# Performance work log

Hardware: AMD Instinct MI355X
Metric: run time of the kernel (lower is better)

## Reference

```python
import jax, jax.numpy as jnp
import numpy as np
from jax import lax

B, TIN, N, TOUT, C = 8, 168, 1500, 24, 16
EMB, ALPHA, BETA, TOPK, DEPTH = 16, 1.5, 0.2, 12, 2
KERNELS = (2, 3, 6, 7)


def setup_inputs() -> dict:
    key = jax.random.key(0)
    ks = jax.random.split(key, 32)
    def rn(k, shape, scale=0.1):
        return jax.random.normal(k, shape, jnp.float32) * scale
    inp = {"x": jax.random.normal(ks[0], (B, TIN, N, 1), jnp.float32)}
    inp["pw"], inp["pb"] = rn(ks[1], (C, 1)), rn(ks[2], (C,))
    branch = C // len(KERNELS)
    for i, k in enumerate(KERNELS):
        inp[f"tw{k}"] = rn(ks[3 + 2 * i], (branch, C, 1, k))
        inp[f"tb{k}"] = rn(ks[4 + 2 * i], (branch,))
    inp["e1"], inp["e2"] = rn(ks[11], (N, EMB), 1.0), rn(ks[12], (N, EMB), 1.0)
    inp["gw1"], inp["gb1"] = rn(ks[13], (EMB, EMB)), rn(ks[14], (EMB,))
    inp["gw2"], inp["gb2"] = rn(ks[15], (EMB, EMB)), rn(ks[16], (EMB,))
    inp["mw"], inp["mb"] = rn(ks[17], (C, (DEPTH + 1) * C)), rn(ks[18], (C,))
    inp["rw1"], inp["rb1"] = rn(ks[19], (C, C)), rn(ks[20], (C,))
    inp["rw2"], inp["rb2"] = rn(ks[21], (TOUT, C)), rn(ks[22], (TOUT,))
    return inp


def _conv1x1(h, w, b):
    # h: [B, Cin, N, T], w: [Cout, Cin], b: [Cout]
    return jnp.einsum('bint,oi->bont', h, w) + b[None, :, None, None]


def _forward(x, pw, pb, tw2, tb2, tw3, tb3, tw6, tb6, tw7, tb7,
             e1, e2, gw1, gb1, gw2, gb2, mw, mb, rw1, rb1, rw2, rb2):
    h = jnp.transpose(x, (0, 3, 2, 1))                      # [B,1,N,TIN]
    h = _conv1x1(h, pw, pb)                                 # [B,C,N,TIN]
    # dilated inception: branches with kernels (2,3,6,7), truncate to shortest
    tlen = TIN - max(KERNELS) + 1
    outs = []
    for w, b in ((tw2, tb2), (tw3, tb3), (tw6, tb6), (tw7, tb7)):
        o = lax.conv_general_dilated(h, w, (1, 1), 'VALID',
                                     dimension_numbers=('NCHW', 'OIHW', 'NCHW'))
        outs.append(o[..., -tlen:] + b[None, :, None, None])
    h = jax.nn.relu(jnp.concatenate(outs, axis=1))          # [B,C,N,tlen]
    # adaptive top-k graph learning
    m1 = jnp.tanh(ALPHA * (e1 @ gw1 + gb1))
    m2 = jnp.tanh(ALPHA * (e2 @ gw2 + gb2))
    a = jax.nn.relu(jnp.tanh(ALPHA * (m1 @ m2.T - m2 @ m1.T)))  # [N,N]
    _, idx = lax.top_k(a, TOPK)
    mask = jnp.zeros((N, N), jnp.float32).at[jnp.arange(N)[:, None], idx].set(1.0)
    adj = a * mask
    # mix-hop graph convolution with row-normalized (A + I)
    adj = adj + jnp.eye(N, dtype=jnp.float32)
    adj = adj / jnp.sum(adj, axis=1, keepdims=True)
    hin = h
    hops = [h]
    for _ in range(DEPTH):
        h = BETA * hin + (1.0 - BETA) * jnp.einsum('bcwt,vw->bcvt', h, adj)
        hops.append(h)
    ho = jnp.concatenate(hops, axis=1)                      # [B,(D+1)C,N,tlen]
    h = jax.nn.relu(_conv1x1(ho, mw, mb))                   # [B,C,N,tlen]
    # dropout -> identity at inference
    r = jax.nn.relu(_conv1x1(h, rw1, rb1))
    y = _conv1x1(r, rw2, rb2)                               # [B,TOUT,N,tlen]
    return jnp.mean(y, axis=-1)                             # [B,TOUT,N]


def reference(x, pw, pb, tw2, tb2, tw3, tb3, tw6, tb6, tw7, tb7,
              e1, e2, gw1, gb1, gw2, gb2, mw, mb, rw1, rb1, rw2, rb2):
    return _forward(x, pw, pb, tw2, tb2, tw3, tb3, tw6, tb6, tw7, tb7,
                    e1, e2, gw1, gb1, gw2, gb2, mw, mb, rw1, rb1, rw2, rb2)
```

## Files before the change

kernel.cpp:

```cpp
#include <hip/hip_runtime.h>

#define BB 8
#define TIN 168
#define NN 1500
#define TOUTC 24
#define TLEN 162
#define NG 32
#define NTH 768
#define SN 2
#define TOPKK 12
#define NTILE 94
#define NPAD 1504

#define OFF_M1   0
#define OFF_M2   24000
#define OFF_EW   48000
#define OFF_EB   48112
#define OFF_ADJW 48128
#define OFF_ADJI 67628
#define OFF_FR   87128
#define OFF_S16  88664
#define OFF_PART 280664

typedef __attribute__((ext_vector_type(8))) short short8;
typedef __attribute__((ext_vector_type(4))) float v4f;

__device__ __forceinline__ unsigned short f2bf(float f) {
    unsigned int u = __float_as_uint(f);
    unsigned int r = (u + 0x7fffu + ((u >> 16) & 1u)) >> 16;
    return (unsigned short)r;
}
__device__ __forceinline__ unsigned int pack2(float lo, float hi) {
    return (unsigned int)f2bf(lo) | ((unsigned int)f2bf(hi) << 16);
}
__device__ __forceinline__ float unlo(unsigned int u) { return __uint_as_float(u << 16); }
__device__ __forceinline__ float unhi(unsigned int u) { return __uint_as_float(u & 0xffff0000u); }
__device__ __forceinline__ float bf2f(unsigned short s) { return __uint_as_float(((unsigned int)s) << 16); }

__device__ __forceinline__ short8 as_s8(uint4 u) { union { uint4 a; short8 b; } c; c.a = u; return c.b; }
__device__ __forceinline__ uint4 zf_u4(v4f f)    { union { v4f a; uint4 b; } c; c.a = f; return c.b; }

__global__ __launch_bounds__(256) void prep_kernel(
    const float* __restrict__ e1, const float* __restrict__ e2,
    const float* __restrict__ gw1, const float* __restrict__ gb1,
    const float* __restrict__ gw2, const float* __restrict__ gb2,
    const float* __restrict__ pw, const float* __restrict__ pb,
    const float* __restrict__ tw2, const float* __restrict__ tb2,
    const float* __restrict__ tw3, const float* __restrict__ tb3,
    const float* __restrict__ tw6, const float* __restrict__ tb6,
    const float* __restrict__ tw7, const float* __restrict__ tb7,
    const float* __restrict__ mw, const float* __restrict__ rw1,
    float* __restrict__ ws)
{
    int n = blockIdx.x * blockDim.x + threadIdx.x;
    if (n < NN) {
        float a1[16], a2[16];
        #pragma unroll
        for (int o = 0; o < 16; ++o) { a1[o] = gb1[o]; a2[o] = gb2[o]; }
        #pragma unroll
        for (int i = 0; i < 16; ++i) {
            float u = e1[n*16+i], v = e2[n*16+i];
            #pragma unroll
            for (int o = 0; o < 16; ++o) {
                a1[o] += u * gw1[i*16+o];
                a2[o] += v * gw2[i*16+o];
            }
        }
        #pragma unroll
        for (int o = 0; o < 16; ++o) {
            ws[OFF_M1 + n*16+o] = tanhf(1.5f*a1[o]);
            ws[OFF_M2 + n*16+o] = tanhf(1.5f*a2[o]);
        }
    }
    if (blockIdx.x == 0 && threadIdx.x < 16) {
        int c = threadIdx.x;
        int br = c >> 2, oc = c & 3;
        const float* tw; const float* tb; int k;
        if (br == 0)      { tw = tw2; tb = tb2; k = 2; }
        else if (br == 1) { tw = tw3; tb = tb3; k = 3; }
        else if (br == 2) { tw = tw6; tb = tb6; k = 6; }
        else              { tw = tw7; tb = tb7; k = 7; }
        for (int d = 0; d < 7; ++d) ws[OFF_EW + c*7 + d] = 0.f;
        float ebv = tb[oc];
        for (int j = 0; j < k; ++j) {
            float s = 0.f, sb = 0.f;
            for (int ic = 0; ic < 16; ++ic) {
                float w = tw[(oc*16+ic)*k + j];
                s  += w * pw[ic];
                sb += w * pb[ic];
            }
            ws[OFF_EW + c*7 + (7-k+j)] = s;
            ebv += sb;
        }
        ws[OFF_EB + c] = ebv;
    }
    if (blockIdx.x == 1 && threadIdx.x < 64) {
        int lane = threadIdx.x;
        int m = lane & 15, q = lane >> 4;
        unsigned short* frw = (unsigned short*)(ws + OFF_FR);
        for (int mat = 0; mat < 3; ++mat) {
            for (int j = 0; j < 8; ++j) {
                int k = q*8 + j;
                float s;
                if (mat == 0) s = (k < 16) ? mw[m*48+k] + 0.2f*(mw[m*48+16+k] + mw[m*48+32+k])
                                           : 0.8f*mw[m*48+16+(k-16)] + 0.16f*mw[m*48+32+(k-16)];
                else if (mat == 1) s = (k < 16) ? 0.64f*mw[m*48+32+k] : 0.f;
                else               s = (k < 16) ? rw1[m*16+k] : 0.f;
                unsigned short hi = f2bf(s);
                unsigned short lo = f2bf(s - bf2f(hi));
                frw[(mat*2+0)*512 + lane*8 + j] = hi;
                frw[(mat*2+1)*512 + lane*8 + j] = lo;
            }
        }
    }
}

__global__ __launch_bounds__(256) void graph_kernel(
    const float* __restrict__ m1, const float* __restrict__ m2,
    float* __restrict__ adjw, int* __restrict__ adji)
{
    int v = blockIdx.x;
    int tid = threadIdx.x;
    __shared__ float wv4[4];
    __shared__ int   wi4[4];
    __shared__ int   bcast_i;
    __shared__ float m1v[16], m2v[16];
    if (tid < 16) { m1v[tid] = m1[v*16+tid]; m2v[tid] = m2[v*16+tid]; }
    __syncthreads();
    const float4* m1f = (const float4*)m1;
    const float4* m2f = (const float4*)m2;
    float sreg[6];
    #pragma unroll
    for (int u = 0; u < 6; ++u) {
        int j = tid + 256*u;
        float a = -1.f;
        if (j < NN) {
            float d = 0.f;
            #pragma unroll
            for (int q = 0; q < 4; ++q) {
                float4 r2 = m2f[j*4+q];
                float4 r1 = m1f[j*4+q];
                d += m1v[4*q+0]*r2.x - m2v[4*q+0]*r1.x;
                d += m1v[4*q+1]*r2.y - m2v[4*q+1]*r1.y;
                d += m1v[4*q+2]*r2.z - m2v[4*q+2]*r1.z;
                d += m1v[4*q+3]*r2.w - m2v[4*q+3]*r1.w;
            }
            float t = tanhf(1.5f*d);
            a = t > 0.f ? t : 0.f;
        }
        sreg[u] = a;
    }
    float lb = -1.f; int li = NN;
    #pragma unroll
    for (int u = 0; u < 6; ++u) {
        int j = tid + 256*u;
        if (j < NN && sreg[u] > lb) { lb = sreg[u]; li = j; }
    }
    const int wid = tid >> 6;
    for (int it = 0; it < TOPKK; ++it) {
        float bv = lb; int bi = li;
        #pragma unroll
        for (int off = 32; off > 0; off >>= 1) {
            float ov = __shfl_down(bv, off);
            int   oi = __shfl_down(bi, off);
            if (ov > bv || (ov == bv && oi < bi)) { bv = ov; bi = oi; }
        }
        if ((tid & 63) == 0) { wv4[wid] = bv; wi4[wid] = bi; }
        __syncthreads();
        if (tid == 0) {
            #pragma unroll
            for (int w = 1; w < 4; ++w) {
                float ov = wv4[w]; int oi = wi4[w];
                if (ov > bv || (ov == bv && oi < bi)) { bv = ov; bi = oi; }
            }
            adjw[v*13+it] = bv;
            adji[v*13+it] = bi;
            bcast_i = bi;
        }
        __syncthreads();
        int win = bcast_i;
        if (li == win) {
            #pragma unroll
            for (int u = 0; u < 6; ++u)
                if (tid + 256*u == win) sreg[u] = -1.f;
            lb = -1.f; li = NN;
            #pragma unroll
            for (int u = 0; u < 6; ++u) {
                int j = tid + 256*u;
                if (j < NN && sreg[u] > lb) { lb = sreg[u]; li = j; }
            }
        }
    }
    if (tid == 0) {
        float s = 1.f;
        #pragma unroll
        for (int it = 0; it < TOPKK; ++it) s += adjw[v*13+it];
        float inv = 1.f/s;
        #pragma unroll
        for (int it = 0; it < TOPKK; ++it) adjw[v*13+it] *= inv;
        adji[v*13+12] = v;
        adjw[v*13+12] = inv;
    }
}

__device__ __forceinline__ short8 ldfrag(const unsigned short* fr, int plane, int lane) {
    const uint4* p = (const uint4*)(fr + plane*512);
    return as_s8(p[lane]);
}

__global__ __launch_bounds__(NTH, 3) void main_kernel(
    const float* __restrict__ x,
    const float* __restrict__ ew, const float* __restrict__ eb,
    const float* __restrict__ adjw, const int* __restrict__ adji,
    const unsigned short* __restrict__ fr,
    float* __restrict__ part,
    const float* __restrict__ mb, const float* __restrict__ rb1)
{
    __shared__ uint4 feat[4][NPAD];
    __shared__ uint4 qp2[2][NPAD];

    const int tid = threadIdx.x;
    const int lane = tid & 63;
    const int wid = tid >> 6;
    const int b = blockIdx.x >> 5;
    const int g = blockIdx.x & 31;
    const int t0 = (g*TLEN) >> 5;
    const int t1 = ((g+1)*TLEN) >> 5;
    float* partBG = part + (size_t)(b*NG + g)*NN*16;

    for (int t = t0; t < t1; ++t) {
        #pragma unroll 1
        for (int s = 0; s < SN; ++s) {
            int v = tid + NTH*s;
            if (v < NN) {
                float xv[7];
                #pragma unroll
                for (int d = 0; d < 7; ++d) xv[d] = x[(b*TIN + t + d)*NN + v];
                float h[16];
                #pragma unroll
                for (int c = 0; c < 16; ++c) {
                    float a = eb[c];
                    #pragma unroll
                    for (int d = 0; d < 7; ++d) a += ew[c*7+d]*xv[d];
                    h[c] = a > 0.f ? a : 0.f;
                }
                feat[0][v] = make_uint4(pack2(h[0],h[1]), pack2(h[2],h[3]), pack2(h[4],h[5]), pack2(h[6],h[7]));
                feat[1][v] = make_uint4(pack2(h[8],h[9]), pack2(h[10],h[11]), pack2(h[12],h[13]), pack2(h[14],h[15]));
            }
        }
        __syncthreads();
        #pragma unroll 1
        for (int s = 0; s < SN; ++s) {
            int v = tid + NTH*s;
            if (v < NN) {
                float u1[16];
                #pragma unroll
                for (int c = 0; c < 16; ++c) u1[c] = 0.f;
                int base = v*13;
                #pragma unroll
                for (int j = 0; j < 13; ++j) {
                    int nb = adji[base+j];
                    float w = adjw[base+j];
                    uint4 b0 = feat[0][nb], b1 = feat[1][nb];
                    unsigned int uu[8] = {b0.x,b0.y,b0.z,b0.w,b1.x,b1.y,b1.z,b1.w};
                    #pragma unroll
                    for (int i = 0; i < 8; ++i) { u1[2*i] += w*unlo(uu[i]); u1[2*i+1] += w*unhi(uu[i]); }
                }
                feat[2][v] = make_uint4(pack2(u1[0],u1[1]), pack2(u1[2],u1[3]), pack2(u1[4],u1[5]), pack2(u1[6],u1[7]));
                feat[3][v] = make_uint4(pack2(u1[8],u1[9]), pack2(u1[10],u1[11]), pack2(u1[12],u1[13]), pack2(u1[14],u1[15]));
            }
        }
        __syncthreads();
        {
            short8 a1h = ldfrag(fr, 0, lane), a1l = ldfrag(fr, 1, lane);
            short8 a2h = ldfrag(fr, 2, lane), a2l = ldfrag(fr, 3, lane);
            const int n0 = lane & 15, q = lane >> 4;
            ushort4* qpH = (ushort4*)qp2;
            #pragma unroll 1
            for (int T = wid; T < NTILE; T += 12) {
                int n = T*16 + n0;
                short8 bf  = as_s8(feat[q][n]);
                short8 b2f = as_s8(feat[2 + (q & 1)][n]);
                v4f z = {0.f,0.f,0.f,0.f}, p = {0.f,0.f,0.f,0.f};
                z = __builtin_amdgcn_mfma_f32_16x16x32_bf16(a1h, bf, z, 0, 0, 0);
                z = __builtin_amdgcn_mfma_f32_16x16x32_bf16(a1l, bf, z, 0, 0, 0);
                p = __builtin_amdgcn_mfma_f32_16x16x32_bf16(a2h, b2f, p, 0, 0, 0);
                p = __builtin_amdgcn_mfma_f32_16x16x32_bf16(a2l, b2f, p, 0, 0, 0);
                feat[q][n] = zf_u4(z);
                ushort4 pp;
                pp.x = f2bf(p[0]); pp.y = f2bf(p[1]); pp.z = f2bf(p[2]); pp.w = f2bf(p[3]);
                qpH[(q >> 1)*(NPAD*2) + n*2 + (q & 1)] = pp;
            }
        }
        __syncthreads();
        #pragma unroll 1
        for (int s = 0; s < SN; ++s) {
            int v = tid + NTH*s;
            if (v < NN) {
                float y[16];
                #pragma unroll
                for (int qq = 0; qq < 4; ++qq) {
                    uint4 zz = feat[qq][v];
                    y[qq*4+0] = mb[qq*4+0] + __uint_as_float(zz.x);
                    y[qq*4+1] = mb[qq*4+1] + __uint_as_float(zz.y);
                    y[qq*4+2] = mb[qq*4+2] + __uint_as_float(zz.z);
                    y[qq*4+3] = mb[qq*4+3] + __uint_as_float(zz.w);
                }
                int base = v*13;
                #pragma unroll
                for (int j = 0; j < 13; ++j) {
                    int nb = adji[base+j];
                    float w = adjw[base+j];
                    uint4 p0 = qp2[0][nb], p1 = qp2[1][nb];
                    unsigned int uu[8] = {p0.x,p0.y,p0.z,p0.w,p1.x,p1.y,p1.z,p1.w};
                    #pragma unroll
                    for (int i = 0; i < 8; ++i) { y[2*i] += w*unlo(uu[i]); y[2*i+1] += w*unhi(uu[i]); }
                }
                #pragma unroll
                for (int o = 0; o < 16; ++o) y[o] = y[o] > 0.f ? y[o] : 0.f;
                feat[0][v] = make_uint4(pack2(y[0],y[1]), pack2(y[2],y[3]), pack2(y[4],y[5]), pack2(y[6],y[7]));
                feat[1][v] = make_uint4(pack2(y[8],y[9]), pack2(y[10],y[11]), pack2(y[12],y[13]), pack2(y[14],y[15]));
                feat[2][v] = make_uint4(0,0,0,0);
                feat[3][v] = make_uint4(0,0,0,0);
            }
        }
        __syncthreads();
        {
            short8 a3h = ldfrag(fr, 4, lane), a3l = ldfrag(fr, 5, lane);
            const int n0 = lane & 15, q = lane >> 4;
            float rb[4];
            #pragma unroll
            for (int r = 0; r < 4; ++r) rb[r] = rb1[q*4+r];
            #pragma unroll 1
            for (int T = wid; T < NTILE; T += 12) {
                int n = T*16 + n0;
                short8 bf = as_s8(feat[q][n]);
                v4f acc = {0.f,0.f,0.f,0.f};
                acc = __builtin_amdgcn_mfma_f32_16x16x32_bf16(a3h, bf, acc, 0, 0, 0);
                acc = __builtin_amdgcn_mfma_f32_16x16x32_bf16(a3l, bf, acc, 0, 0, 0);
                if (n < NN) {
                    float r0 = acc[0]+rb[0], r1 = acc[1]+rb[1], r2 = acc[2]+rb[2], r3 = acc[3]+rb[3];
                    r0 = r0 > 0.f ? r0 : 0.f;  r1 = r1 > 0.f ? r1 : 0.f;
                    r2 = r2 > 0.f ? r2 : 0.f;  r3 = r3 > 0.f ? r3 : 0.f;
                    float4* pp = (float4*)(partBG + (size_t)n*16 + q*4);
                    if (t == t0) {
                        *pp = make_float4(r0, r1, r2, r3);
                    } else {
                        float4 o = *pp;
                        *pp = make_float4(o.x+r0, o.y+r1, o.z+r2, o.w+r3);
                    }
                }
            }
        }
        __syncthreads();
    }
}

__global__ __launch_bounds__(256) void reduce1_kernel(const float* __restrict__ part,
                                                      float* __restrict__ s16buf)
{
    int idx = blockIdx.x*256 + threadIdx.x;
    if (idx >= BB*NN*16) return;
    int c = idx & 15;
    int rest = idx >> 4;
    int v = rest % NN;
    int b = rest / NN;
    float s = 0.f;
    #pragma unroll
    for (int g = 0; g < NG; ++g)
        s += part[((size_t)(b*NG + g)*NN + v)*16 + c];
    s16buf[idx] = s * (1.0f/TLEN);
}

__global__ __launch_bounds__(256) void reduce2_kernel(const float* __restrict__ s16buf,
                                                      const float* __restrict__ rw2,
                                                      const float* __restrict__ rb2,
                                                      float* __restrict__ out)
{
    int idx = blockIdx.x*256 + threadIdx.x;
    if (idx >= BB*NN) return;
    int v = idx % NN;
    int b = idx / NN;
    const float4* sp = (const float4*)(s16buf + (size_t)idx*16);
    float4 s0 = sp[0], s1 = sp[1], s2 = sp[2], s3 = sp[3];
    float s16[16] = {s0.x,s0.y,s0.z,s0.w, s1.x,s1.y,s1.z,s1.w,
                     s2.x,s2.y,s2.z,s2.w, s3.x,s3.y,s3.z,s3.w};
    #pragma unroll
    for (int o = 0; o < TOUTC; ++o) {
        float a = rb2[o];
        #pragma unroll
        for (int c = 0; c < 16; ++c) a += rw2[o*16+c]*s16[c];
        out[(b*TOUTC + o)*NN + v] = a;
    }
}

extern "C" void kernel_launch(void* const* d_in, const int* in_sizes, int n_in,
                              void* d_out, int out_size, void* d_ws, size_t ws_size,
                              hipStream_t stream)
{
    const float* x   = (const float*)d_in[0];
    const float* pw  = (const float*)d_in[1];
    const float* pb  = (const float*)d_in[2];
    const float* tw2 = (const float*)d_in[3];
    const float* tb2 = (const float*)d_in[4];
    const float* tw3 = (const float*)d_in[5];
    const float* tb3 = (const float*)d_in[6];
    const float* tw6 = (const float*)d_in[7];
    const float* tb6 = (const float*)d_in[8];
    const float* tw7 = (const float*)d_in[9];
    const float* tb7 = (const float*)d_in[10];
    const float* e1  = (const float*)d_in[11];
    const float* e2  = (const float*)d_in[12];
    const float* gw1 = (const float*)d_in[13];
    const float* gb1 = (const float*)d_in[14];
    const float* gw2 = (const float*)d_in[15];
    const float* gb2 = (const float*)d_in[16];
    const float* mw  = (const float*)d_in[17];
    const float* mb  = (const float*)d_in[18];
    const float* rw1 = (const float*)d_in[19];
    const float* rb1 = (const float*)d_in[20];
    const float* rw2 = (const float*)d_in[21];
    const float* rb2 = (const float*)d_in[22];
    float* ws  = (float*)d_ws;
    float* out = (float*)d_out;

    prep_kernel<<<(NN + 255)/256, 256, 0, stream>>>(e1,e2,gw1,gb1,gw2,gb2,pw,pb,
                                                    tw2,tb2,tw3,tb3,tw6,tb6,tw7,tb7,
                                                    mw, rw1, ws);
    graph_kernel<<<NN, 256, 0, stream>>>(ws + OFF_M1, ws + OFF_M2,
                                         ws + OFF_ADJW, (int*)ws + OFF_ADJI);
    main_kernel<<<BB*NG, NTH, 0, stream>>>(x, ws + OFF_EW, ws + OFF_EB,
                                           ws + OFF_ADJW, (const int*)ws + OFF_ADJI,
                                           (const unsigned short*)(ws + OFF_FR),
                                           ws + OFF_PART, mb, rb1);
    reduce1_kernel<<<(BB*NN*16 + 255)/256, 256, 0, stream>>>(ws + OFF_PART, ws + OFF_S16);
    reduce2_kernel<<<(BB*NN + 255)/256, 256, 0, stream>>>(ws + OFF_S16, rw2, rb2, out);
}
```

Measured before the change: 299.7 us.

## Fuse second hop into final MFMA tile loop and double-buffer input features

Restructures the main kernel's per-timestep pipeline. The input-projection features for the next timestep are computed into an alternate shared buffer, and the second-hop aggregation is folded into the tile loop that feeds the final MFMA. This removes one per-vertex pass and one block barrier per timestep and overlaps the next step's x loads with current work. The z and p intermediates are now stored as bf16, which adds rounding error. Separately, the graph kernel reads transposed embedding copies so its loads coalesce, at the cost of two extra workspace arrays written in the prep kernel.

```diff
diff --git a/kernel.cpp b/kernel.cpp
--- a/kernel.cpp
+++ b/kernel.cpp
@@ -14,13 +14,15 @@
 
 #define OFF_M1   0
 #define OFF_M2   24000
-#define OFF_EW   48000
-#define OFF_EB   48112
-#define OFF_ADJW 48128
-#define OFF_ADJI 67628
-#define OFF_FR   87128
-#define OFF_S16  88664
-#define OFF_PART 280664
+#define OFF_M1T  48000
+#define OFF_M2T  72000
+#define OFF_EW   96000
+#define OFF_EB   96112
+#define OFF_ADJW 96128
+#define OFF_ADJI 115628
+#define OFF_FR   135128
+#define OFF_S16  136664
+#define OFF_PART 328664
 
 typedef __attribute__((ext_vector_type(8))) short short8;
 typedef __attribute__((ext_vector_type(4))) float v4f;
@@ -38,7 +40,6 @@
 __device__ __forceinline__ float bf2f(unsigned short s) { return __uint_as_float(((unsigned int)s) << 16); }
 
 __device__ __forceinline__ short8 as_s8(uint4 u) { union { uint4 a; short8 b; } c; c.a = u; return c.b; }
-__device__ __forceinline__ uint4 zf_u4(v4f f)    { union { v4f a; uint4 b; } c; c.a = f; return c.b; }
 
 __global__ __launch_bounds__(256) void prep_kernel(
     const float* __restrict__ e1, const float* __restrict__ e2,
@@ -68,8 +69,12 @@
         }
         #pragma unroll
         for (int o = 0; o < 16; ++o) {
-            ws[OFF_M1 + n*16+o] = tanhf(1.5f*a1[o]);
-            ws[OFF_M2 + n*16+o] = tanhf(1.5f*a2[o]);
+            float t1v = tanhf(1.5f*a1[o]);
+            float t2v = tanhf(1.5f*a2[o]);
+            ws[OFF_M1 + n*16+o] = t1v;
+            ws[OFF_M2 + n*16+o] = t2v;
+            ws[OFF_M1T + o*NN + n] = t1v;
+            ws[OFF_M2T + o*NN + n] = t2v;
         }
     }
     if (blockIdx.x == 0 && threadIdx.x < 16) {
@@ -117,6 +122,7 @@
 
 __global__ __launch_bounds__(256) void graph_kernel(
     const float* __restrict__ m1, const float* __restrict__ m2,
+    const float* __restrict__ m1T, const float* __restrict__ m2T,
     float* __restrict__ adjw, int* __restrict__ adji)
 {
     int v = blockIdx.x;
@@ -127,8 +133,6 @@
     __shared__ float m1v[16], m2v[16];
     if (tid < 16) { m1v[tid] = m1[v*16+tid]; m2v[tid] = m2[v*16+tid]; }
     __syncthreads();
-    const float4* m1f = (const float4*)m1;
-    const float4* m2f = (const float4*)m2;
     float sreg[6];
     #pragma unroll
     for (int u = 0; u < 6; ++u) {
@@ -137,14 +141,8 @@
         if (j < NN) {
             float d = 0.f;
             #pragma unroll
-            for (int q = 0; q < 4; ++q) {
-                float4 r2 = m2f[j*4+q];
-                float4 r1 = m1f[j*4+q];
-                d += m1v[4*q+0]*r2.x - m2v[4*q+0]*r1.x;
-                d += m1v[4*q+1]*r2.y - m2v[4*q+1]*r1.y;
-                d += m1v[4*q+2]*r2.z - m2v[4*q+2]*r1.z;
-                d += m1v[4*q+3]*r2.w - m2v[4*q+3]*r1.w;
-            }
+            for (int i = 0; i < 16; ++i)
+                d += m1v[i]*m2T[i*NN+j] - m2v[i]*m1T[i*NN+j];
             float t = tanhf(1.5f*d);
             a = t > 0.f ? t : 0.f;
         }
@@ -216,8 +214,7 @@
     float* __restrict__ part,
     const float* __restrict__ mb, const float* __restrict__ rb1)
 {
-    __shared__ uint4 feat[4][NPAD];
-    __shared__ uint4 qp2[2][NPAD];
+    __shared__ uint4 feat[6][NPAD];
 
     const int tid = threadIdx.x;
     const int lane = tid & 63;
@@ -226,29 +223,35 @@
     const int g = blockIdx.x & 31;
     const int t0 = (g*TLEN) >> 5;
     const int t1 = ((g+1)*TLEN) >> 5;
+    const int n0 = lane & 15, q = lane >> 4;
     float* partBG = part + (size_t)(b*NG + g)*NN*16;
 
+    #pragma unroll 1
+    for (int s = 0; s < SN; ++s) {
+        int v = tid + NTH*s;
+        if (v < NN) {
+            float xv[7];
+            #pragma unroll
+            for (int d = 0; d < 7; ++d) xv[d] = x[(b*TIN + t0 + d)*NN + v];
+            float h[16];
+            #pragma unroll
+            for (int c = 0; c < 16; ++c) {
+                float a = eb[c];
+                #pragma unroll
+                for (int d = 0; d < 7; ++d) a += ew[c*7+d]*xv[d];
+                h[c] = a > 0.f ? a : 0.f;
+            }
+            feat[0][v] = make_uint4(pack2(h[0],h[1]), pack2(h[2],h[3]), pack2(h[4],h[5]), pack2(h[6],h[7]));
+            feat[1][v] = make_uint4(pack2(h[8],h[9]), pack2(h[10],h[11]), pack2(h[12],h[13]), pack2(h[14],h[15]));
+        }
+    }
+    __syncthreads();
+
     for (int t = t0; t < t1; ++t) {
-        #pragma unroll 1
-        for (int s = 0; s < SN; ++s) {
-            int v = tid + NTH*s;
-            if (v < NN) {
-                float xv[7];
-                #pragma unroll
-                for (int d = 0; d < 7; ++d) xv[d] = x[(b*TIN + t + d)*NN + v];
-                float h[16];
-                #pragma unroll
-                for (int c = 0; c < 16; ++c) {
-                    float a = eb[c];
-                    #pragma unroll
-                    for (int d = 0; d < 7; ++d) a += ew[c*7+d]*xv[d];
-                    h[c] = a > 0.f ? a : 0.f;
-                }
-                feat[0][v] = make_uint4(pack2(h[0],h[1]), pack2(h[2],h[3]), pack2(h[4],h[5]), pack2(h[6],h[7]));
-                feat[1][v] = make_uint4(pack2(h[8],h[9]), pack2(h[10],h[11]), pack2(h[12],h[13]), pack2(h[14],h[15]));
-            }
-        }
-        __syncthreads();
+        const int par = (t - t0) & 1;
+        const int hc = par ? 4 : 0;
+        const int hn = par ? 0 : 4;
+
         #pragma unroll 1
         for (int s = 0; s < SN; ++s) {
             int v = tid + NTH*s;
@@ -261,7 +264,7 @@
                 for (int j = 0; j < 13; ++j) {
                     int nb = adji[base+j];
                     float w = adjw[base+j];
-                    uint4 b0 = feat[0][nb], b1 = feat[1][nb];
+                    uint4 b0 = feat[hc][nb], b1 = feat[hc+1][nb];
                     unsigned int uu[8] = {b0.x,b0.y,b0.z,b0.w,b1.x,b1.y,b1.z,b1.w};
                     #pragma unroll
                     for (int i = 0; i < 8; ++i) { u1[2*i] += w*unlo(uu[i]); u1[2*i+1] += w*unhi(uu[i]); }
@@ -271,75 +274,85 @@
             }
         }
         __syncthreads();
+
         {
             short8 a1h = ldfrag(fr, 0, lane), a1l = ldfrag(fr, 1, lane);
             short8 a2h = ldfrag(fr, 2, lane), a2l = ldfrag(fr, 3, lane);
-            const int n0 = lane & 15, q = lane >> 4;
-            ushort4* qpH = (ushort4*)qp2;
+            ushort4* zH = (ushort4*)feat[hc + (q >> 1)];
+            ushort4* pH = (ushort4*)feat[2  + (q >> 1)];
             #pragma unroll 1
             for (int T = wid; T < NTILE; T += 12) {
                 int n = T*16 + n0;
-                short8 bf  = as_s8(feat[q][n]);
+                short8 bf  = as_s8(feat[(q < 2) ? (hc + q) : q][n]);
                 short8 b2f = as_s8(feat[2 + (q & 1)][n]);
                 v4f z = {0.f,0.f,0.f,0.f}, p = {0.f,0.f,0.f,0.f};
                 z = __builtin_amdgcn_mfma_f32_16x16x32_bf16(a1h, bf, z, 0, 0, 0);
                 z = __builtin_amdgcn_mfma_f32_16x16x32_bf16(a1l, bf, z, 0, 0, 0);
                 p = __builtin_amdgcn_mfma_f32_16x16x32_bf16(a2h, b2f, p, 0, 0, 0);
                 p = __builtin_amdgcn_mfma_f32_16x16x32_bf16(a2l, b2f, p, 0, 0, 0);
-                feat[q][n] = zf_u4(z);
-                ushort4 pp;
-                pp.x = f2bf(p[0]); pp.y = f2bf(p[1]); pp.z = f2bf(p[2]); pp.w = f2bf(p[3]);
-                qpH[(q >> 1)*(NPAD*2) + n*2 + (q & 1)] = pp;
+                ushort4 zz; zz.x = f2bf(z[0]); zz.y = f2bf(z[1]); zz.z = f2bf(z[2]); zz.w = f2bf(z[3]);
+                ushort4 pp; pp.x = f2bf(p[0]); pp.y = f2bf(p[1]); pp.z = f2bf(p[2]); pp.w = f2bf(p[3]);
+                zH[n*2 + (q & 1)] = zz;
+                pH[n*2 + (q & 1)] = pp;
             }
         }
         __syncthreads();
-        #pragma unroll 1
-        for (int s = 0; s < SN; ++s) {
-            int v = tid + NTH*s;
-            if (v < NN) {
-                float y[16];
-                #pragma unroll
-                for (int qq = 0; qq < 4; ++qq) {
-                    uint4 zz = feat[qq][v];
-                    y[qq*4+0] = mb[qq*4+0] + __uint_as_float(zz.x);
-                    y[qq*4+1] = mb[qq*4+1] + __uint_as_float(zz.y);
-                    y[qq*4+2] = mb[qq*4+2] + __uint_as_float(zz.z);
-                    y[qq*4+3] = mb[qq*4+3] + __uint_as_float(zz.w);
+
+        if (t + 1 < t1) {
+            #pragma unroll 1
+            for (int s = 0; s < SN; ++s) {
+                int v = tid + NTH*s;
+                if (v < NN) {
+                    float xv[7];
+                    #pragma unroll
+                    for (int d = 0; d < 7; ++d) xv[d] = x[(b*TIN + (t+1) + d)*NN + v];
+                    float h[16];
+                    #pragma unroll
+                    for (int c = 0; c < 16; ++c) {
+                        float a = eb[c];
+                        #pragma unroll
+                        for (int d = 0; d < 7; ++d) a += ew[c*7+d]*xv[d];
+                        h[c] = a > 0.f ? a : 0.f;
+                    }
+                    feat[hn][v]   = make_uint4(pack2(h[0],h[1]), pack2(h[2],h[3]), pack2(h[4],h[5]), pack2(h[6],h[7]));
+                    feat[hn+1][v] = make_uint4(pack2(h[8],h[9]), pack2(h[10],h[11]), pack2(h[12],h[13]), pack2(h[14],h[15]));
                 }
-                int base = v*13;
+            }
+        }
+        {
+            short8 a3h = ldfrag(fr, 4, lane), a3l = ldfrag(fr, 5, lane);
+            float mbq[4], rbq[4];
+            #pragma unroll
+            for (int r = 0; r < 4; ++r) { mbq[r] = mb[q*4+r]; rbq[r] = rb1[q*4+r]; }
+            ushort4* zH = (ushort4*)feat[hc + (q >> 1)];
+            const ushort4* pH = (const ushort4*)feat[2 + (q >> 1)];
+            #pragma unroll 1
+            for (int T = wid; T < NTILE; T += 12) {
+                int n = T*16 + n0;
+                ushort4 zz = zH[n*2 + (q & 1)];
+                float y0 = mbq[0] + bf2f(zz.x);
+                float y1 = mbq[1] + bf2f(zz.y);
+                float y2 = mbq[2] + bf2f(zz.z);
+                float y3 = mbq[3] + bf2f(zz.w);
+                int base = (n < NN ? n : NN-1) * 13;
                 #pragma unroll
                 for (int j = 0; j < 13; ++j) {
                     int nb = adji[base+j];
                     float w = adjw[base+j];
-                    uint4 p0 = qp2[0][nb], p1 = qp2[1][nb];
-                    unsigned int uu[8] = {p0.x,p0.y,p0.z,p0.w,p1.x,p1.y,p1.z,p1.w};
-                    #pragma unroll
-                    for (int i = 0; i < 8; ++i) { y[2*i] += w*unlo(uu[i]); y[2*i+1] += w*unhi(uu[i]); }
+                    ushort4 ps = pH[nb*2 + (q & 1)];
+                    y0 += w*bf2f(ps.x); y1 += w*bf2f(ps.y);
+                    y2 += w*bf2f(ps.z); y3 += w*bf2f(ps.w);
                 }
-                #pragma unroll
-                for (int o = 0; o < 16; ++o) y[o] = y[o] > 0.f ? y[o] : 0.f;
-                feat[0][v] = make_uint4(pack2(y[0],y[1]), pack2(y[2],y[3]), pack2(y[4],y[5]), pack2(y[6],y[7]));
-                feat[1][v] = make_uint4(pack2(y[8],y[9]), pack2(y[10],y[11]), pack2(y[12],y[13]), pack2(y[14],y[15]));
-                feat[2][v] = make_uint4(0,0,0,0);
-                feat[3][v] = make_uint4(0,0,0,0);
-            }
-        }
-        __syncthreads();
-        {
-            short8 a3h = ldfrag(fr, 4, lane), a3l = ldfrag(fr, 5, lane);
-            const int n0 = lane & 15, q = lane >> 4;
-            float rb[4];
-            #pragma unroll
-            for (int r = 0; r < 4; ++r) rb[r] = rb1[q*4+r];
-            #pragma unroll 1
-            for (int T = wid; T < NTILE; T += 12) {
-                int n = T*16 + n0;
-                short8 bf = as_s8(feat[q][n]);
+                y0 = y0 > 0.f ? y0 : 0.f;  y1 = y1 > 0.f ? y1 : 0.f;
+                y2 = y2 > 0.f ? y2 : 0.f;  y3 = y3 > 0.f ? y3 : 0.f;
+                ushort4 yy; yy.x = f2bf(y0); yy.y = f2bf(y1); yy.z = f2bf(y2); yy.w = f2bf(y3);
+                zH[n*2 + (q & 1)] = yy;
+                short8 bfY = as_s8(feat[(q < 2) ? (hc + q) : q][n]);
                 v4f acc = {0.f,0.f,0.f,0.f};
-                acc = __builtin_amdgcn_mfma_f32_16x16x32_bf16(a3h, bf, acc, 0, 0, 0);
-                acc = __builtin_amdgcn_mfma_f32_16x16x32_bf16(a3l, bf, acc, 0, 0, 0);
+                acc = __builtin_amdgcn_mfma_f32_16x16x32_bf16(a3h, bfY, acc, 0, 0, 0);
+                acc = __builtin_amdgcn_mfma_f32_16x16x32_bf16(a3l, bfY, acc, 0, 0, 0);
                 if (n < NN) {
-                    float r0 = acc[0]+rb[0], r1 = acc[1]+rb[1], r2 = acc[2]+rb[2], r3 = acc[3]+rb[3];
+                    float r0 = acc[0]+rbq[0], r1 = acc[1]+rbq[1], r2 = acc[2]+rbq[2], r3 = acc[3]+rbq[3];
                     r0 = r0 > 0.f ? r0 : 0.f;  r1 = r1 > 0.f ? r1 : 0.f;
                     r2 = r2 > 0.f ? r2 : 0.f;  r3 = r3 > 0.f ? r3 : 0.f;
                     float4* pp = (float4*)(partBG + (size_t)n*16 + q*4);
@@ -428,6 +441,7 @@
                                                     tw2,tb2,tw3,tb3,tw6,tb6,tw7,tb7,
                                                     mw, rw1, ws);
     graph_kernel<<<NN, 256, 0, stream>>>(ws + OFF_M1, ws + OFF_M2,
+                                         ws + OFF_M1T, ws + OFF_M2T,
                                          ws + OFF_ADJW, (int*)ws + OFF_ADJI);
     main_kernel<<<BB*NG, NTH, 0, stream>>>(x, ws + OFF_EW, ws + OFF_EB,
                                            ws + OFF_ADJW, (const int*)ws + OFF_ADJI,
```

New measurement: 299.0 us. About the same (-0.2%).
